# Optimization experiments

Hardware: AMD Instinct MI355X
Metric: run time of the kernel (lower is better)

Reference implementation:

```python
import jax, jax.numpy as jnp
import numpy as np

EMB = 1024
NH = 8
HD = EMB // NH
EPS = 1e-6


def setup_inputs() -> dict:
    key = jax.random.key(0)
    ks = jax.random.split(key, 6)
    B, S = 2, 2048
    q = jax.random.normal(ks[0], (B, S, EMB), jnp.float32)
    k = jax.random.normal(ks[1], (B, S, EMB), jnp.float32)
    v = jax.random.normal(ks[2], (B, S, EMB), jnp.float32)
    # gate Dense params: input dim 3*EMB (concat of q,k,v), output NH
    igate_kernel = jax.random.normal(ks[3], (3 * EMB, NH), jnp.float32) * 0.02
    igate_bias = jax.random.normal(ks[4], (NH,), jnp.float32) * 0.1
    fgate_kernel = jax.random.normal(ks[5], (3 * EMB, NH), jnp.float32) * 0.02
    fgate_bias = jnp.linspace(3.0, 6.0, NH).astype(jnp.float32)  # bias_linspace_init
    return dict(q=q, k=k, v=v, igate_kernel=igate_kernel, igate_bias=igate_bias,
                fgate_kernel=fgate_kernel, fgate_bias=fgate_bias)


def _mlstm_head(q, k, v, ig, fg):
    # q,k,v: (S, DH); ig, fg: (S, 1) gate preactivations for this head
    S, DH = q.shape
    log_fg = jax.nn.log_sigmoid(fg)                                   # (S,1)
    cs = jnp.concatenate([jnp.zeros((1, 1), q.dtype),
                          jnp.cumsum(log_fg, axis=0)], axis=0)        # (S+1,1)
    fg_mat_full = cs - cs.T                                           # (S+1,S+1): cumsum_i - cumsum_j
    ltr = jnp.tril(jnp.ones((S, S), bool))
    log_fg_matrix = jnp.where(ltr, fg_mat_full[1:, 1:], -jnp.inf)     # causal decay
    log_D = log_fg_matrix + ig.T                                      # (S,S)
    max_log_D = jnp.max(log_D, axis=-1, keepdims=True)                # row-wise stabilizer
    D = jnp.exp(log_D - max_log_D)
    qk = q @ (k.T / jnp.sqrt(jnp.asarray(DH, q.dtype)))               # (S,S)
    C = qk * D
    normalizer = jnp.maximum(jnp.abs(C.sum(-1, keepdims=True)), jnp.exp(-max_log_D))
    return (C / (normalizer + EPS)) @ v                               # (S,DH)


def reference(q, k, v, igate_kernel, igate_bias, fgate_kernel, fgate_bias):
    B, S, H = q.shape
    x = jnp.concatenate([q, k, v], axis=-1)                           # (B,S,3H)
    ig = x @ igate_kernel + igate_bias                                # (B,S,NH)
    fg = x @ fgate_kernel + fgate_bias                                # (B,S,NH)
    qh = q.reshape(B, S, NH, HD).swapaxes(1, 2)                       # (B,NH,S,DH)
    kh = k.reshape(B, S, NH, HD).swapaxes(1, 2)
    vh = v.reshape(B, S, NH, HD).swapaxes(1, 2)
    igp = ig.swapaxes(1, 2)[..., None]                                # (B,NH,S,1)
    fgp = fg.swapaxes(1, 2)[..., None]
    h = jax.vmap(jax.vmap(_mlstm_head))(qh, kh, vh, igp, fgp)         # (B,NH,S,DH)
    # RMSNorm over head_dim (last axis), computed in fp32
    hf = h.astype(jnp.float32)
    h = (hf * jax.lax.rsqrt(jnp.mean(jnp.square(hf), axis=-1, keepdims=True) + 1e-6)).astype(h.dtype)
    return h.swapaxes(1, 2).reshape(B, S, H)
```

## Files before the change

### kernel.cpp

```cpp
#include <hip/hip_runtime.h>

#define S_LEN 2048
#define EMB_D 1024
#define QK_SCALE 0.08838834764831845f
#define RS128 11.313708498984761f
#define LOG2E 1.4426950408889634f

typedef _Float16 f16;
typedef f16 f16x8 __attribute__((ext_vector_type(8)));
typedef float f32x4 __attribute__((ext_vector_type(4)));
typedef unsigned short ushort_t;

typedef const __attribute__((address_space(1))) void gvoid;
typedef __attribute__((address_space(3))) void lvoid;

__device__ __forceinline__ ushort_t f2h(float x) {
    return __builtin_bit_cast(ushort_t, (f16)x);
}
__device__ __forceinline__ unsigned pk2h(float a, float b) {
    return __builtin_bit_cast(unsigned, __builtin_amdgcn_cvt_pkrtz(a, b));
}
__device__ __forceinline__ void gl_lds(const void* g, void* l) {
    __builtin_amdgcn_global_load_lds((gvoid*)g, (lvoid*)l, 16, 0, 0);
}

__global__ __launch_bounds__(256) void ktransW(const float* __restrict__ igk,
                                               const float* __restrict__ fgk,
                                               ushort_t* __restrict__ Wf) {
    int gid = blockIdx.x * 256 + threadIdx.x;
    int ks_g = gid >> 6, lane = gid & 63;
    int n = lane & 15, lg = lane >> 4;
    int src = ks_g >> 5, rem = ks_g & 31;
    int hemb = rem >> 2, ks = rem & 3;
    int e0 = src * 1024 + hemb * 128 + ks * 32 + lg * 8;
    float scale = (src == 0) ? RS128 : 1.0f;
    const float* col = (n < 8) ? igk : fgk;
    int nn = n & 7;
    union { ushort_t u[8]; uint4 v4; } P;
    #pragma unroll
    for (int e = 0; e < 8; ++e) P.u[e] = f2h(col[(size_t)(e0 + e) * 8 + nn] * scale);
    *(uint4*)((char*)Wf + ks_g * 1024 + lane * 16) = P.v4;
}

__global__ __launch_bounds__(256) void kprep(const float* __restrict__ q,
                                             const float* __restrict__ k,
                                             const float* __restrict__ v,
                                             const ushort_t* __restrict__ Wf,
                                             const float* __restrict__ igb,
                                             const float* __restrict__ fgb,
                                             ushort_t* __restrict__ Qf,
                                             ushort_t* __restrict__ Kf,
                                             ushort_t* __restrict__ Vt,
                                             float* __restrict__ igp_t,
                                             float* __restrict__ fgp_t) {
    __shared__ __align__(16) ushort_t xs[3 * 8 * 16 * 128];
    __shared__ __align__(16) float red[4][64][4];
    const int blk = blockIdx.x;
    const int b = blk >> 7, strip = blk & 127;
    const int s0 = strip * 16;
    const int tile = strip >> 2, subrow = (strip & 3) * 16;
    const int t = threadIdx.x;
    const int w = t >> 6, lane = t & 63;
    const int ll = lane & 15, lg = lane >> 4;

    #pragma unroll
    for (int src = 0; src < 3; ++src) {
        const float* sp = (src == 0 ? q : src == 1 ? k : v) + ((size_t)b * S_LEN + s0) * EMB_D;
        float scale = (src == 0) ? QK_SCALE : 1.0f;
        #pragma unroll
        for (int i = 0; i < 16; ++i) {
            int f = i * 256 + t;
            int r = f >> 8, c4 = f & 255;
            int col = c4 * 4;
            float4 x = *(const float4*)(sp + (size_t)r * EMB_D + col);
            ushort4 H;
            H.x = f2h(x.x * scale); H.y = f2h(x.y * scale);
            H.z = f2h(x.z * scale); H.w = f2h(x.w * scale);
            int hh = col >> 7, d0 = col & 127;
            *(ushort4*)((char*)xs + ((((src * 8 + hh) * 16 + r) * 256 + d0 * 2) ^ ((r & 7) << 4))) = H;
            if (src < 2) {
                char* dst = (char*)(src ? Kf : Qf) + ((size_t)(b * 8 + hh) * 32 + tile) * 16384;
                *(ushort4*)(dst + (((subrow + r) * 256 + d0 * 2) ^ ((r & 7) << 4))) = H;
            }
        }
    }
    __syncthreads();
    #pragma unroll
    for (int it = 0; it < 8; ++it) {
        int item = it * 256 + t;
        int d = item & 127, jo = (item >> 7) & 1, hh = item >> 8;
        union { ushort_t u[8]; uint4 v4; } P;
        #pragma unroll
        for (int e = 0; e < 8; ++e) {
            int r = jo * 8 + e;
            P.u[e] = *(const ushort_t*)((const char*)xs
                       + ((((16 + hh) * 16 + r) * 256 + d * 2) ^ ((r & 7) << 4)));
        }
        char* vd = (char*)Vt + ((size_t)(b * 8 + hh) * 32 + tile) * 16384
                 + ((strip & 3) * 2 + jo) * 2048 + d * 16;
        *(uint4*)vd = P.v4;
    }
    f32x4 acc = {0.f, 0.f, 0.f, 0.f};
    for (int ri = w * 6; ri < w * 6 + 6; ++ri) {
        int src = ri >> 3, hemb = ri & 7;
        #pragma unroll
        for (int ks = 0; ks < 4; ++ks) {
            f16x8 af = *(const f16x8*)((const char*)xs
                        + ((((src * 8 + hemb) * 16 + ll) * 256 + ks * 64 + lg * 16) ^ ((ll & 7) << 4)));
            f16x8 bf = *(const f16x8*)((const char*)Wf + (src * 32 + hemb * 4 + ks) * 1024 + lane * 16);
            acc = __builtin_amdgcn_mfma_f32_16x16x32_f16(af, bf, acc, 0, 0, 0);
        }
    }
    *(f32x4*)&red[w][lane][0] = acc;
    __syncthreads();
    if (w == 0) {
        f32x4 o2 = acc;
        #pragma unroll
        for (int ww = 1; ww < 4; ++ww) o2 += *(const f32x4*)&red[ww][lane][0];
        float bias = (ll < 8) ? igb[ll] : fgb[ll - 8];
        float* dst = (ll < 8) ? igp_t : fgp_t;
        size_t ob = (size_t)(b * 8 + (ll & 7)) * S_LEN + s0 + lg * 4;
        #pragma unroll
        for (int r = 0; r < 4; ++r) dst[ob + r] = o2[r] + bias;
    }
}

__global__ __launch_bounds__(64) void kscan(const float* __restrict__ igp_t,
                                            const float* __restrict__ fgp_t,
                                            float* __restrict__ a_w,
                                            float* __restrict__ pm_w,
                                            float* __restrict__ nf_w) {
    const int bh = blockIdx.x;
    const int l = threadIdx.x;
    const int base = bh * S_LEN + l * 32;
    float lf[32];
    #pragma unroll
    for (int i = 0; i < 8; ++i) {
        float4 fg = *(const float4*)(fgp_t + base + i * 4);
        float* p = &lf[i * 4];
        p[0] = fminf(fg.x, 0.f) - log1pf(__expf(-fabsf(fg.x)));
        p[1] = fminf(fg.y, 0.f) - log1pf(__expf(-fabsf(fg.y)));
        p[2] = fminf(fg.z, 0.f) - log1pf(__expf(-fabsf(fg.z)));
        p[3] = fminf(fg.w, 0.f) - log1pf(__expf(-fabsf(fg.w)));
    }
    #pragma unroll
    for (int i = 1; i < 32; ++i) lf[i] += lf[i - 1];
    float tot = lf[31];
    #pragma unroll
    for (int d = 1; d < 64; d <<= 1) {
        float n = __shfl_up(tot, d, 64);
        if (l >= d) tot += n;
    }
    float excl = tot - lf[31];
    float cs[32], a[32];
    #pragma unroll
    for (int i = 0; i < 8; ++i) {
        float4 ig = *(const float4*)(igp_t + base + i * 4);
        float iv[4] = {ig.x, ig.y, ig.z, ig.w};
        #pragma unroll
        for (int e = 0; e < 4; ++e) {
            int idx = i * 4 + e;
            cs[idx] = excl + lf[idx];
            a[idx] = iv[e] - cs[idx];
            a_w[base + idx] = a[idx] * LOG2E;
        }
    }
    float am[32];
    am[0] = a[0];
    #pragma unroll
    for (int i = 1; i < 32; ++i) am[i] = fmaxf(am[i - 1], a[i]);
    float mtot = am[31];
    #pragma unroll
    for (int d = 1; d < 64; d <<= 1) {
        float n = __shfl_up(mtot, d, 64);
        if (l >= d) mtot = fmaxf(mtot, n);
    }
    float exm = __shfl_up(mtot, 1, 64);
    if (l == 0) exm = -INFINITY;
    #pragma unroll
    for (int i = 0; i < 32; ++i) {
        float pmv = fmaxf(exm, am[i]);
        pm_w[base + i] = pmv * LOG2E;
        nf_w[base + i] = __expf(-(cs[i] + pmv));
    }
}

__global__ __launch_bounds__(512, 2) void kmain(const ushort_t* __restrict__ Qf,
                                                const ushort_t* __restrict__ Kf,
                                                const ushort_t* __restrict__ Vt,
                                                const float* __restrict__ a_w,
                                                const float* __restrict__ pm_w,
                                                const float* __restrict__ nf_w,
                                                float* __restrict__ out) {
    __shared__ __align__(16) ushort_t Kbuf[2][2][8192];
    __shared__ __align__(16) ushort_t Csh[2][4096];
    __shared__ float redL[2][2][64];

    const int blk = blockIdx.x;
    const int bh = blk & 15;
    const int pair = blk >> 4;
    const int b = bh >> 3, h = bh & 7;
    const int t = threadIdx.x;
    const int w = t >> 6, lane = t & 63;
    const int g = w >> 2, wl = w & 3;
    const int wr = wl >> 1, wc = wl & 1;
    const int lg = lane >> 4, ll = lane & 15;
    const int sw = (ll & 7) << 4;

    const char* q_b = (const char*)Qf + (size_t)bh * 524288;
    const char* k_b = (const char*)Kf + (size_t)bh * 524288;
    const char* v_b = (const char*)Vt + (size_t)bh * 524288;
    const float* aw = a_w + bh * S_LEN;

    float* accX = (float*)&Kbuf[0][0][0];
    float* rsX  = (float*)&Csh[0][0];

    for (int half = 0; half < 2; ++half) {
        const int rt = half ? (31 - pair) : pair;
        const int row0 = rt * 64;
        const int nss = (rt >> 1) + 1;
        __syncthreads();

        const char* qt = q_b + (size_t)rt * 16384;
        f16x8 qf[2][4];
        #pragma unroll
        for (int ib = 0; ib < 2; ++ib) {
            int row = 32 * wr + 16 * ib + ll;
            #pragma unroll
            for (int kk = 0; kk < 4; ++kk)
                qf[ib][kk] = *(const f16x8*)(qt + ((row * 256 + lg * 16 + kk * 64) ^ ((row & 7) << 4)));
        }
        float pm2[2];
        #pragma unroll
        for (int ib = 0; ib < 2; ++ib)
            pm2[ib] = pm_w[bh * S_LEN + row0 + 32 * wr + 16 * ib + ll];

        f16x8 bvA[2][4], bvB[2][4];
        f32x4 avA[2] = {{0.f,0.f,0.f,0.f},{0.f,0.f,0.f,0.f}};
        f32x4 avB[2] = {{0.f,0.f,0.f,0.f},{0.f,0.f,0.f,0.f}};
        if (g <= rt) {
            const char* kt = k_b + (size_t)g * 16384;
            #pragma unroll
            for (int i = 0; i < 4; ++i) {
                int o = (wl * 4 + i) * 1024 + lane * 16;
                gl_lds(kt + o, (char*)&Kbuf[g][0][0] + o);
            }
            const char* vt = v_b + (size_t)g * 16384;
            #pragma unroll
            for (int kk = 0; kk < 2; ++kk)
                #pragma unroll
                for (int vf = 0; vf < 4; ++vf)
                    bvA[kk][vf] = *(const f16x8*)(vt + (kk * 4 + lg) * 2048 + (64 * wc + 16 * vf + ll) * 16);
            #pragma unroll
            for (int jb = 0; jb < 2; ++jb)
                avA[jb] = *(const f32x4*)(aw + g * 64 + 32 * wc + 16 * jb + 4 * lg);
        }
        asm volatile("s_waitcnt vmcnt(0)" ::: "memory");
        __builtin_amdgcn_s_barrier();

        f32x4 zero4 = {0.f, 0.f, 0.f, 0.f};
        f32x4 accO[2][4];
        #pragma unroll
        for (int ib = 0; ib < 2; ++ib)
            #pragma unroll
            for (int vf = 0; vf < 4; ++vf) accO[ib][vf] = zero4;
        float rs[2] = {0.f, 0.f};

        auto STEP = [&](int ssv, int P, f16x8 (&bvC)[2][4], f16x8 (&bvN)[2][4],
                        f32x4 (&avC)[2], f32x4 (&avN)[2]) {
            const int myct = 2 * ssv + g;
            const int nxct = myct + 2;
            if (nxct <= rt) {
                const char* kt = k_b + (size_t)nxct * 16384;
                #pragma unroll
                for (int i = 0; i < 4; ++i) {
                    int o = (wl * 4 + i) * 1024 + lane * 16;
                    gl_lds(kt + o, (char*)&Kbuf[g][P ^ 1][0] + o);
                }
                const char* vt = v_b + (size_t)nxct * 16384;
                #pragma unroll
                for (int kk = 0; kk < 2; ++kk)
                    #pragma unroll
                    for (int vf = 0; vf < 4; ++vf)
                        bvN[kk][vf] = *(const f16x8*)(vt + (kk * 4 + lg) * 2048 + (64 * wc + 16 * vf + ll) * 16);
                #pragma unroll
                for (int jb = 0; jb < 2; ++jb)
                    avN[jb] = *(const f32x4*)(aw + nxct * 64 + 32 * wc + 16 * jb + 4 * lg);
            }
            const bool act = (myct <= rt);
            if (act) {
                const char* kl = (const char*)&Kbuf[g][P][0];
                f32x4 accST[2][2];
                accST[0][0] = zero4; accST[0][1] = zero4;
                accST[1][0] = zero4; accST[1][1] = zero4;
                __builtin_amdgcn_s_setprio(1);
                #pragma unroll
                for (int kk = 0; kk < 4; ++kk) {
                    f16x8 kf0 = *(const f16x8*)(kl + (((32 * wc + ll) * 256 + lg * 16 + kk * 64) ^ sw));
                    f16x8 kf1 = *(const f16x8*)(kl + (((32 * wc + 16 + ll) * 256 + lg * 16 + kk * 64) ^ sw));
                    accST[0][0] = __builtin_amdgcn_mfma_f32_16x16x32_f16(kf0, qf[0][kk], accST[0][0], 0, 0, 0);
                    accST[0][1] = __builtin_amdgcn_mfma_f32_16x16x32_f16(kf0, qf[1][kk], accST[0][1], 0, 0, 0);
                    accST[1][0] = __builtin_amdgcn_mfma_f32_16x16x32_f16(kf1, qf[0][kk], accST[1][0], 0, 0, 0);
                    accST[1][1] = __builtin_amdgcn_mfma_f32_16x16x32_f16(kf1, qf[1][kk], accST[1][1], 0, 0, 0);
                }
                __builtin_amdgcn_s_setprio(0);
                const bool diag = (myct == rt);
                #pragma unroll
                for (int jb = 0; jb < 2; ++jb) {
                    #pragma unroll
                    for (int ib = 0; ib < 2; ++ib) {
                        int il = 32 * wr + 16 * ib + ll;
                        float cv[4];
                        #pragma unroll
                        for (int r = 0; r < 4; ++r) {
                            int jl = 32 * wc + 16 * jb + 4 * lg + r;
                            float x = accST[jb][ib][r] * exp2f(avC[jb][r] - pm2[ib]);
                            if (diag && jl > il) x = 0.f;
                            rs[ib] += x;
                            cv[r] = x;
                        }
                        int off = (il * 128 + (32 * wc + 16 * jb + 4 * lg) * 2) ^ ((il & 7) << 4);
                        uint2 pk2; pk2.x = pk2h(cv[0], cv[1]); pk2.y = pk2h(cv[2], cv[3]);
                        *(uint2*)((char*)&Csh[g][0] + off) = pk2;
                    }
                }
            }
            asm volatile("s_waitcnt lgkmcnt(0)" ::: "memory");
            __builtin_amdgcn_s_barrier();
            if (act) {
                __builtin_amdgcn_s_setprio(1);
                #pragma unroll
                for (int kk = 0; kk < 2; ++kk)
                    #pragma unroll
                    for (int ib = 0; ib < 2; ++ib) {
                        int rowA = 32 * wr + 16 * ib + ll;
                        f16x8 pa = *(const f16x8*)((const char*)&Csh[g][0]
                                                   + ((rowA * 128 + lg * 16 + kk * 64) ^ ((rowA & 7) << 4)));
                        #pragma unroll
                        for (int vf = 0; vf < 4; ++vf)
                            accO[ib][vf] = __builtin_amdgcn_mfma_f32_16x16x32_f16(pa, bvC[kk][vf], accO[ib][vf], 0, 0, 0);
                    }
                __builtin_amdgcn_s_setprio(0);
            }
            asm volatile("s_waitcnt vmcnt(0)" ::: "memory");
            __builtin_amdgcn_s_barrier();
        };

        for (int ss = 0; ss < nss; ss += 2) {
            STEP(ss, 0, bvA, bvB, avA, avB);
            if (ss + 1 < nss) STEP(ss + 1, 1, bvB, bvA, avB, avA);
        }

        __syncthreads();
        const int li = wl * 64 + lane;
        const int lsw = (li & 7) << 2;
        if (g == 1) {
            #pragma unroll
            for (int ib = 0; ib < 2; ++ib)
                #pragma unroll
                for (int vf = 0; vf < 4; ++vf)
                    *(f32x4*)&accX[(li * 32 + (ib * 4 + vf) * 4) ^ lsw] = accO[ib][vf];
            rsX[li * 2 + 0] = rs[0];
            rsX[li * 2 + 1] = rs[1];
        }
        __syncthreads();
        if (g == 0) {
            #pragma unroll
            for (int ib = 0; ib < 2; ++ib)
                #pragma unroll
                for (int vf = 0; vf < 4; ++vf)
                    accO[ib][vf] += *(const f32x4*)&accX[(li * 32 + (ib * 4 + vf) * 4) ^ lsw];
            rs[0] += rsX[li * 2 + 0];
            rs[1] += rsX[li * 2 + 1];
            #pragma unroll
            for (int ib = 0; ib < 2; ++ib) {
                rs[ib] += __shfl_xor(rs[ib], 16);
                rs[ib] += __shfl_xor(rs[ib], 32);
            }
            if (lg == 0) {
                redL[0][wc][32 * wr + ll] = rs[0];
                redL[0][wc][32 * wr + 16 + ll] = rs[1];
            }
        }
        __syncthreads();
        if (g == 0) {
            float invn[2][4];
            #pragma unroll
            for (int ib = 0; ib < 2; ++ib)
                #pragma unroll
                for (int r = 0; r < 4; ++r) {
                    int il = 32 * wr + 16 * ib + 4 * lg + r;
                    float tot = redL[0][0][il] + redL[0][1][il];
                    float nf = nf_w[bh * S_LEN + row0 + il];
                    invn[ib][r] = 1.0f / (fmaxf(fabsf(tot), nf) + 1e-6f);
                }
            float ssq[2][4] = {{0.f, 0.f, 0.f, 0.f}, {0.f, 0.f, 0.f, 0.f}};
            #pragma unroll
            for (int ib = 0; ib < 2; ++ib)
                #pragma unroll
                for (int vf = 0; vf < 4; ++vf)
                    #pragma unroll
                    for (int r = 0; r < 4; ++r) {
                        float hv = accO[ib][vf][r] * invn[ib][r];
                        ssq[ib][r] += hv * hv;
                    }
            #pragma unroll
            for (int m = 1; m < 16; m <<= 1)
                #pragma unroll
                for (int ib = 0; ib < 2; ++ib)
                    #pragma unroll
                    for (int r = 0; r < 4; ++r) ssq[ib][r] += __shfl_xor(ssq[ib][r], m);
            if (ll == 0) {
                #pragma unroll
                for (int ib = 0; ib < 2; ++ib)
                    #pragma unroll
                    for (int r = 0; r < 4; ++r)
                        redL[1][wc][32 * wr + 16 * ib + 4 * lg + r] = ssq[ib][r];
            }
            __builtin_amdgcn_s_barrier();
            float* ob = out + ((size_t)b * S_LEN + row0) * EMB_D + h * 128;
            #pragma unroll
            for (int ib = 0; ib < 2; ++ib)
                #pragma unroll
                for (int r = 0; r < 4; ++r) {
                    int il = 32 * wr + 16 * ib + 4 * lg + r;
                    float sst = redL[1][0][il] + redL[1][1][il];
                    float scl = rsqrtf(sst * (1.0f / 128.0f) + 1e-6f) * invn[ib][r];
                    #pragma unroll
                    for (int vf = 0; vf < 4; ++vf) {
                        int d = 64 * wc + 16 * vf + ll;
                        ob[(size_t)il * EMB_D + d] = accO[ib][vf][r] * scl;
                    }
                }
        } else {
            __builtin_amdgcn_s_barrier();
        }
    }
}

extern "C" void kernel_launch(void* const* d_in, const int* in_sizes, int n_in,
                              void* d_out, int out_size, void* d_ws, size_t ws_size,
                              hipStream_t stream) {
    const float* q   = (const float*)d_in[0];
    const float* k   = (const float*)d_in[1];
    const float* v   = (const float*)d_in[2];
    const float* igk = (const float*)d_in[3];
    const float* igb = (const float*)d_in[4];
    const float* fgk = (const float*)d_in[5];
    const float* fgb = (const float*)d_in[6];
    float* out = (float*)d_out;

    char* W = (char*)d_ws;
    ushort_t* Wf   = (ushort_t*)(W);
    float* igp_t   = (float*)(W + 98304);
    float* fgp_t   = (float*)(W + 229376);
    float* a_w     = (float*)(W + 360448);
    float* pm_w    = (float*)(W + 491520);
    float* nf_w    = (float*)(W + 622592);
    ushort_t* Qf   = (ushort_t*)(W + 753664);
    ushort_t* Kf   = (ushort_t*)(W + 753664 + 1 * 8388608ull);
    ushort_t* Vt   = (ushort_t*)(W + 753664 + 2 * 8388608ull);

    ktransW<<<24, 256, 0, stream>>>(igk, fgk, Wf);
    kprep<<<256, 256, 0, stream>>>(q, k, v, Wf, igb, fgb, Qf, Kf, Vt, igp_t, fgp_t);
    kscan<<<16, 64, 0, stream>>>(igp_t, fgp_t, a_w, pm_w, nf_w);
    kmain<<<256, 512, 0, stream>>>(Qf, Kf, Vt, a_w, pm_w, nf_w, out);
}
```

Baseline: 96.48 us.

## Stage V tiles through LDS with async loads instead of register prefetch

V tiles are now double-buffered in shared memory via global_load_lds alongside K, instead of being prefetched into registers. The manually unrolled two-step lambda becomes a plain loop with parity selection, and the occupancy hint in launch_bounds is dropped. The intent is to cut VGPR pressure and let the async LDS path carry V. In exchange it adds 64KB of LDS per block, which may prevent two blocks per CU, plus extra LDS reads in the PV MFMA loop and possible bank conflicts, since V reads are not swizzled.

Result: faster. 77.80 us (-19.4%).

```diff
diff --git a/kernel.cpp b/kernel.cpp
--- a/kernel.cpp
+++ b/kernel.cpp
@@ -185,14 +185,15 @@
     }
 }
 
-__global__ __launch_bounds__(512, 2) void kmain(const ushort_t* __restrict__ Qf,
-                                                const ushort_t* __restrict__ Kf,
-                                                const ushort_t* __restrict__ Vt,
-                                                const float* __restrict__ a_w,
-                                                const float* __restrict__ pm_w,
-                                                const float* __restrict__ nf_w,
-                                                float* __restrict__ out) {
+__global__ __launch_bounds__(512) void kmain(const ushort_t* __restrict__ Qf,
+                                             const ushort_t* __restrict__ Kf,
+                                             const ushort_t* __restrict__ Vt,
+                                             const float* __restrict__ a_w,
+                                             const float* __restrict__ pm_w,
+                                             const float* __restrict__ nf_w,
+                                             float* __restrict__ out) {
     __shared__ __align__(16) ushort_t Kbuf[2][2][8192];
+    __shared__ __align__(16) ushort_t Vbuf[2][2][8192];
     __shared__ __align__(16) ushort_t Csh[2][4096];
     __shared__ float redL[2][2][64];
 
@@ -235,22 +236,17 @@
         for (int ib = 0; ib < 2; ++ib)
             pm2[ib] = pm_w[bh * S_LEN + row0 + 32 * wr + 16 * ib + ll];
 
-        f16x8 bvA[2][4], bvB[2][4];
         f32x4 avA[2] = {{0.f,0.f,0.f,0.f},{0.f,0.f,0.f,0.f}};
         f32x4 avB[2] = {{0.f,0.f,0.f,0.f},{0.f,0.f,0.f,0.f}};
         if (g <= rt) {
             const char* kt = k_b + (size_t)g * 16384;
+            const char* vt = v_b + (size_t)g * 16384;
             #pragma unroll
             for (int i = 0; i < 4; ++i) {
                 int o = (wl * 4 + i) * 1024 + lane * 16;
                 gl_lds(kt + o, (char*)&Kbuf[g][0][0] + o);
-            }
-            const char* vt = v_b + (size_t)g * 16384;
-            #pragma unroll
-            for (int kk = 0; kk < 2; ++kk)
-                #pragma unroll
-                for (int vf = 0; vf < 4; ++vf)
-                    bvA[kk][vf] = *(const f16x8*)(vt + (kk * 4 + lg) * 2048 + (64 * wc + 16 * vf + ll) * 16);
+                gl_lds(vt + o, (char*)&Vbuf[g][0][0] + o);
+            }
             #pragma unroll
             for (int jb = 0; jb < 2; ++jb)
                 avA[jb] = *(const f32x4*)(aw + g * 64 + 32 * wc + 16 * jb + 4 * lg);
@@ -266,30 +262,32 @@
             for (int vf = 0; vf < 4; ++vf) accO[ib][vf] = zero4;
         float rs[2] = {0.f, 0.f};
 
-        auto STEP = [&](int ssv, int P, f16x8 (&bvC)[2][4], f16x8 (&bvN)[2][4],
-                        f32x4 (&avC)[2], f32x4 (&avN)[2]) {
-            const int myct = 2 * ssv + g;
+        for (int ss = 0; ss < nss; ++ss) {
+            const int p = ss & 1;
+            const int myct = 2 * ss + g;
             const int nxct = myct + 2;
             if (nxct <= rt) {
                 const char* kt = k_b + (size_t)nxct * 16384;
+                const char* vt = v_b + (size_t)nxct * 16384;
                 #pragma unroll
                 for (int i = 0; i < 4; ++i) {
                     int o = (wl * 4 + i) * 1024 + lane * 16;
-                    gl_lds(kt + o, (char*)&Kbuf[g][P ^ 1][0] + o);
-                }
-                const char* vt = v_b + (size_t)nxct * 16384;
-                #pragma unroll
-                for (int kk = 0; kk < 2; ++kk)
-                    #pragma unroll
-                    for (int vf = 0; vf < 4; ++vf)
-                        bvN[kk][vf] = *(const f16x8*)(vt + (kk * 4 + lg) * 2048 + (64 * wc + 16 * vf + ll) * 16);
-                #pragma unroll
-                for (int jb = 0; jb < 2; ++jb)
-                    avN[jb] = *(const f32x4*)(aw + nxct * 64 + 32 * wc + 16 * jb + 4 * lg);
+                    gl_lds(kt + o, (char*)&Kbuf[g][p ^ 1][0] + o);
+                    gl_lds(vt + o, (char*)&Vbuf[g][p ^ 1][0] + o);
+                }
+                if (p == 0) {
+                    #pragma unroll
+                    for (int jb = 0; jb < 2; ++jb)
+                        avB[jb] = *(const f32x4*)(aw + nxct * 64 + 32 * wc + 16 * jb + 4 * lg);
+                } else {
+                    #pragma unroll
+                    for (int jb = 0; jb < 2; ++jb)
+                        avA[jb] = *(const f32x4*)(aw + nxct * 64 + 32 * wc + 16 * jb + 4 * lg);
+                }
             }
             const bool act = (myct <= rt);
             if (act) {
-                const char* kl = (const char*)&Kbuf[g][P][0];
+                const char* kl = (const char*)&Kbuf[g][p][0];
                 f32x4 accST[2][2];
                 accST[0][0] = zero4; accST[0][1] = zero4;
                 accST[1][0] = zero4; accST[1][1] = zero4;
@@ -307,6 +305,9 @@
                 const bool diag = (myct == rt);
                 #pragma unroll
                 for (int jb = 0; jb < 2; ++jb) {
+                    f32x4 av;
+                    #pragma unroll
+                    for (int r = 0; r < 4; ++r) av[r] = (p == 0) ? avA[jb][r] : avB[jb][r];
                     #pragma unroll
                     for (int ib = 0; ib < 2; ++ib) {
                         int il = 32 * wr + 16 * ib + ll;
@@ -314,7 +315,7 @@
                         #pragma unroll
                         for (int r = 0; r < 4; ++r) {
                             int jl = 32 * wc + 16 * jb + 4 * lg + r;
-                            float x = accST[jb][ib][r] * exp2f(avC[jb][r] - pm2[ib]);
+                            float x = accST[jb][ib][r] * exp2f(av[r] - pm2[ib]);
                             if (diag && jl > il) x = 0.f;
                             rs[ib] += x;
                             cv[r] = x;
@@ -328,6 +329,7 @@
             asm volatile("s_waitcnt lgkmcnt(0)" ::: "memory");
             __builtin_amdgcn_s_barrier();
             if (act) {
+                const char* vl = (const char*)&Vbuf[g][p][0];
                 __builtin_amdgcn_s_setprio(1);
                 #pragma unroll
                 for (int kk = 0; kk < 2; ++kk)
@@ -337,18 +339,16 @@
                         f16x8 pa = *(const f16x8*)((const char*)&Csh[g][0]
                                                    + ((rowA * 128 + lg * 16 + kk * 64) ^ ((rowA & 7) << 4)));
                         #pragma unroll
-                        for (int vf = 0; vf < 4; ++vf)
-                            accO[ib][vf] = __builtin_amdgcn_mfma_f32_16x16x32_f16(pa, bvC[kk][vf], accO[ib][vf], 0, 0, 0);
+                        for (int vf = 0; vf < 4; ++vf) {
+                            f16x8 vb2 = *(const f16x8*)(vl + (kk * 4 + lg) * 2048
+                                                        + (64 * wc + 16 * vf + ll) * 16);
+                            accO[ib][vf] = __builtin_amdgcn_mfma_f32_16x16x32_f16(pa, vb2, accO[ib][vf], 0, 0, 0);
+                        }
                     }
                 __builtin_amdgcn_s_setprio(0);
             }
             asm volatile("s_waitcnt vmcnt(0)" ::: "memory");
             __builtin_amdgcn_s_barrier();
-        };
-
-        for (int ss = 0; ss < nss; ss += 2) {
-            STEP(ss, 0, bvA, bvB, avA, avB);
-            if (ss + 1 < nss) STEP(ss + 1, 1, bvB, bvA, avB, avA);
         }
 
         __syncthreads();
```
